# Kernel optimization log

Measured on AMD Instinct MI355X. Metric: run time of the kernel, lower is better.

## Reference

```python
import jax, jax.numpy as jnp
import numpy as np

H = 64        # hidden_dim
A = 21        # N_ACTIONS
B = 262144    # batch size


def setup_inputs() -> dict:
    key = jax.random.key(0)
    ks = jax.random.split(key, 32)

    def w(k, shape):
        fan_in = shape[0]
        return (jax.random.normal(k, shape, jnp.float32) / np.float32(np.sqrt(fan_in)))

    inp = {
        "x": jax.random.normal(ks[0], (B, 2, 2), jnp.float32),
        "b_act1": jax.random.randint(ks[1], (B,), 0, A),
        "b_act2": jax.random.randint(ks[2], (B,), 0, A),
        # enc: Linear(2,H), ReLU, Linear(H,H), ReLU
        "enc_w1": w(ks[3], (2, H)), "enc_b1": jnp.zeros((H,), jnp.float32),
        "enc_w2": w(ks[4], (H, H)), "enc_b2": jnp.zeros((H,), jnp.float32),
        # q_net: Linear(H,H), ReLU, Linear(H,A)
        "q_w1": w(ks[5], (H, H)), "q_b1": jnp.zeros((H,), jnp.float32),
        "q_w2": w(ks[6], (H, A)), "q_b2": jnp.zeros((A,), jnp.float32),
        # v_net: Linear(H,H), ReLU, Linear(H,1)
        "v_w1": w(ks[7], (H, H)), "v_b1": jnp.zeros((H,), jnp.float32),
        "v_w2": w(ks[8], (H, 1)), "v_b2": jnp.zeros((1,), jnp.float32),
        # lin2: Linear(H+A,H), ReLU, Linear(H,H), ReLU, Linear(H,H)
        "l2_w1": w(ks[9], (H + A, H)), "l2_b1": jnp.zeros((H,), jnp.float32),
        "l2_w2": w(ks[10], (H, H)), "l2_b2": jnp.zeros((H,), jnp.float32),
        "l2_w3": w(ks[11], (H, H)), "l2_b3": jnp.zeros((H,), jnp.float32),
        # lin3, lin4
        "l3_w": w(ks[12], (H, H)), "l3_b": jnp.zeros((H,), jnp.float32),
        "l4_w": w(ks[13], (H, A)), "l4_b": jnp.zeros((A,), jnp.float32),
        # q_prime_net: Linear(H,2H) ELU Linear(2H,H) ELU Linear(H,H) ELU Linear(H,1)
        "qp_w1": w(ks[14], (H, 2 * H)), "qp_b1": jnp.zeros((2 * H,), jnp.float32),
        "qp_w2": w(ks[15], (2 * H, H)), "qp_b2": jnp.zeros((H,), jnp.float32),
        "qp_w3": w(ks[16], (H, H)), "qp_b3": jnp.zeros((H,), jnp.float32),
        "qp_w4": w(ks[17], (H, 1)), "qp_b4": jnp.zeros((1,), jnp.float32),
    }
    return inp


def reference(x, b_act1, b_act2,
              enc_w1, enc_b1, enc_w2, enc_b2,
              q_w1, q_b1, q_w2, q_b2,
              v_w1, v_b1, v_w2, v_b2,
              l2_w1, l2_b1, l2_w2, l2_b2, l2_w3, l2_b3,
              l3_w, l3_b, l4_w, l4_b,
              qp_w1, qp_b1, qp_w2, qp_b2, qp_w3, qp_b3, qp_w4, qp_b4):
    relu = jax.nn.relu
    elu = jax.nn.elu

    def enc(z):
        return relu(relu(z @ enc_w1 + enc_b1) @ enc_w2 + enc_b2)

    def q_net(h):
        return relu(h @ q_w1 + q_b1) @ q_w2 + q_b2

    def lin2(e):  # ends with bare Linear (no final activation)
        h = relu(e @ l2_w1 + l2_b1)
        h = relu(h @ l2_w2 + l2_b2)
        return h @ l2_w3 + l2_b3

    def q_prime(z):
        h = elu(z @ qp_w1 + qp_b1)
        h = elu(h @ qp_w2 + qp_b2)
        h = elu(h @ qp_w3 + qp_b3)
        return h @ qp_w4 + qp_b4

    h1 = enc(x[:, 0, :])  # [B,H]
    h2 = enc(x[:, 1, :])
    q1, q2 = q_net(h1), q_net(h2)              # [B,A]
    key2 = jnp.stack([h1, h2], axis=1)          # [B,2,H]
    vtot = relu((h1 + h2) @ v_w1 + v_b1) @ v_w2 + v_b2  # [B,1]

    def joint(act1, act2):
        oh1 = jax.nn.one_hot(act1, A, dtype=h1.dtype)
        oh2 = jax.nn.one_hot(act2, A, dtype=h2.dtype)
        e = jnp.stack([jnp.concatenate([h1, oh1], axis=-1),
                       jnp.concatenate([h2, oh2], axis=-1)], axis=1)  # [B,2,H+A]
        key1 = lin2(e)                              # [B,2,H]
        q = q_prime(key1.mean(axis=1))              # [B,1]
        return key1, q

    key1, joint_qs = joint(b_act1, b_act2)
    a1_max = jnp.argmax(q1, axis=1)
    a2_max = jnp.argmax(q2, axis=1)
    key1_max, joint_max_qs = joint(a1_max, a2_max)

    def q_jt(k1):
        z = key2 + k1.mean(axis=1, keepdims=True) - k1 / 2  # [B,2,H]
        return relu(z @ l3_w + l3_b) @ l4_w + l4_b           # [B,2,A]

    q_jt_alt = q_jt(key1)
    q_jt_max_alt = q_jt(key1_max)

    return (q1, q2, joint_qs, joint_max_qs, vtot, q_jt_alt, q_jt_max_alt)
```

## Files before the change

### kernel.cpp

```cpp
#include <hip/hip_runtime.h>
#include <hip/hip_bf16.h>


#define B_TOT 262144

typedef __bf16 bf16_t;
typedef __bf16 bf16x4 __attribute__((ext_vector_type(4)));
typedef __bf16 bf16x8 __attribute__((ext_vector_type(8)));
typedef float  f32x2  __attribute__((ext_vector_type(2)));
typedef float  f32x4  __attribute__((ext_vector_type(4)));

#define MFMA16(a, b, c) __builtin_amdgcn_mfma_f32_16x16x32_bf16((a), (b), (c), 0, 0, 0)

enum : int {
  OFF_VW1  = 0,
  OFF_L2W1 = 4096,
  OFF_L2W2 = 8192,
  OFF_L2W3 = 12288,
  OFF_L3W  = 16384,
  OFF_L4W  = 20480,
  OFF_QP1  = 22528,
  OFF_QP2  = 30720,
  OFF_QP3  = 38912,
  WS_ELEMS = 43008
};
#define WS_BYTES (WS_ELEMS * 2)

enum : int {
  O_Q1   = 0,
  O_Q2   = 21 * B_TOT,
  O_JQ   = 42 * B_TOT,
  O_JMQ  = 43 * B_TOT,
  O_VT   = 44 * B_TOT,
  O_QJT  = 45 * B_TOT,
  O_QJTM = 87 * B_TOT
};

struct RDesc { const float* src; int K; int N; int NT; int off; };
struct RPack { RDesc d[9]; };

__global__ void repack_kernel(RPack P, bf16_t* __restrict__ ws) {
  RDesc d = P.d[blockIdx.x];
  int n = (d.K >> 5) * d.NT * 512;
  for (int i = threadIdx.x; i < n; i += blockDim.x) {
    int j  = i & 7;
    int l  = (i >> 3) & 63;
    int t  = i >> 9;
    int nt = t % d.NT;
    int kc = t / d.NT;
    int sk = kc * 32 + 16 * (j >> 2) + 4 * (l >> 4) + (j & 3);
    int sn = nt * 16 + (l & 15);
    float v = (sn < d.N) ? d.src[sk * d.N + sn] : 0.0f;
    ws[d.off + i] = (bf16_t)v;
  }
}

struct Args {
  const float* x; const int* a1; const int* a2;
  const float* ew1; const float* eb1; const float* ew2; const float* eb2;
  const float* qw1; const float* qb1; const float* qw2; const float* qb2;
  const float* vw1; const float* vb1; const float* vw2; const float* vb2;
  const float* l2w1; const float* l2b1; const float* l2w2; const float* l2b2;
  const float* l2w3; const float* l2b3;
  const float* l3w;  const float* l3b;  const float* l4w;  const float* l4b;
  const float* qpw1; const float* qpb1; const float* qpw2; const float* qpb2;
  const float* qpw3; const float* qpb3; const float* qpw4; const float* qpb4;
  float* out; const bf16_t* ws;
};

struct __align__(16) SMem {
  unsigned char scr[16896];
  bf16_t h1b[64 * 68];
  bf16_t h2b[64 * 68];
  float  bias[768];
  int    acts[128];
  int    amax[128];
  float  red[64][2];
  int    redi[64][2];
};

__device__ __forceinline__ float eluf(float x) { return x > 0.f ? x : expm1f(x); }

__device__ __forceinline__ void fcA64ip(float* __restrict__ f,
                                        const float* __restrict__ W,
                                        const float* __restrict__ Bv,
                                        bf16_t* __restrict__ hb, int r, int g) {
  f32x2 acc[8];
  const f32x2* Bv2 = (const f32x2*)(Bv + g * 16);
#pragma unroll
  for (int i = 0; i < 8; i++) acc[i] = Bv2[i];
  const f32x2* fr = (const f32x2*)(f + r * 66);
#pragma unroll 1
  for (int hh = 0; hh < 2; hh++) {
    f32x2 in[16];
#pragma unroll
    for (int i = 0; i < 16; i++) in[i] = fr[16 * hh + i];
#pragma unroll 4
    for (int k2 = 0; k2 < 16; k2++) {
      int k = 32 * hh + 2 * k2;
      const f32x2* wr0 = (const f32x2*)(W + k * 64 + g * 16);
      const f32x2* wr1 = (const f32x2*)(W + (k + 1) * 64 + g * 16);
      f32x2 a0 = {in[k2][0], in[k2][0]};
      f32x2 a1 = {in[k2][1], in[k2][1]};
#pragma unroll
      for (int i = 0; i < 8; i++) acc[i] += a0 * wr0[i];
#pragma unroll
      for (int i = 0; i < 8; i++) acc[i] += a1 * wr1[i];
    }
  }
  __syncthreads();
#pragma unroll
  for (int i = 0; i < 8; i++) {
    float v0 = fmaxf(acc[i][0], 0.f), v1 = fmaxf(acc[i][1], 0.f);
    f32x2 v = {v0, v1};
    *(f32x2*)(f + r * 66 + g * 16 + 2 * i) = v;
    if (hb) {
      hb[r * 68 + g * 16 + 2 * i]     = (bf16_t)v0;
      hb[r * 68 + g * 16 + 2 * i + 1] = (bf16_t)v1;
    }
  }
  __syncthreads();
}

template <int NC>
__device__ __forceinline__ void qn2(const float* __restrict__ fin, const float* __restrict__ W21,
                                    const float* __restrict__ Bv, float* __restrict__ qo,
                                    int r, int colbase, float& bv, int& bi) {
  float acc[NC];
#pragma unroll
  for (int i = 0; i < NC; i++) acc[i] = Bv[colbase + i];
  for (int k2 = 0; k2 < 32; k2++) {
    f32x2 a = *(const f32x2*)(fin + r * 66 + 2 * k2);
    const float* wr0 = W21 + (2 * k2) * 21 + colbase;
    const float* wr1 = W21 + (2 * k2 + 1) * 21 + colbase;
#pragma unroll
    for (int i = 0; i < NC; i++) acc[i] = fmaf(a[0], wr0[i], acc[i]);
#pragma unroll
    for (int i = 0; i < NC; i++) acc[i] = fmaf(a[1], wr1[i], acc[i]);
  }
  bv = -3e38f; bi = 0;
#pragma unroll
  for (int i = 0; i < NC; i++) {
    qo[i] = acc[i];
    if (acc[i] > bv) { bv = acc[i]; bi = colbase + i; }
  }
}

template <bool USEWS, int NT, int KC>
__device__ __forceinline__ f32x4 tileT(const bf16x8* __restrict__ WF,
                                       const float* __restrict__ Wp, int N, int woff,
                                       const bf16x8* __restrict__ bin,
                                       const float* __restrict__ bias, int bbase,
                                       int nt, int l, int c, int u) {
  f32x4 a = *(const f32x4*)(bias + bbase + nt * 16 + 4 * u);
#pragma unroll
  for (int kc = 0; kc < KC; kc++) {
    bf16x8 w;
    if constexpr (USEWS) {
      w = WF[(woff >> 3) + (kc * NT + nt) * 64 + l];
    } else {
      int sn = nt * 16 + c;
      if (sn < N) {
#pragma unroll
        for (int j = 0; j < 8; j++)
          w[j] = (bf16_t)Wp[(kc * 32 + 16 * (j >> 2) + 4 * u + (j & 3)) * N + sn];
      } else {
#pragma unroll
        for (int j = 0; j < 8; j++) w[j] = (bf16_t)0.0f;
      }
    }
    a = MFMA16(w, bin[kc], a);
  }
  return a;
}

template <int MODE>
__device__ __forceinline__ bf16x8 pack2(f32x4 t0, f32x4 t1) {
  bf16x8 r;
#pragma unroll
  for (int j = 0; j < 8; j++) {
    float v = (j >> 2) ? t1[j & 3] : t0[j & 3];
    if constexpr (MODE == 1) v = fmaxf(v, 0.f);
    if constexpr (MODE == 2) v = eluf(v);
    r[j] = (bf16_t)v;
  }
  return r;
}

template <bool USEWS>
__global__ __launch_bounds__(256, 3) void qtran_main(Args A) {
  __shared__ SMem sm;
  const int t = threadIdx.x;
  const int wgbase = blockIdx.x * 64;
  const int r = t & 63;
  const int g = __builtin_amdgcn_readfirstlane(t >> 6);

  float* f0 = (float*)sm.scr;

  if (t < 64) {
    sm.bias[t]        = A.vb1[t];
    sm.bias[64 + t]   = A.l2b1[t];
    sm.bias[128 + t]  = A.l2b2[t];
    sm.bias[192 + t]  = A.l2b3[t];
    sm.bias[384 + t]  = A.qpb2[t];
    sm.bias[448 + t]  = A.qpb3[t];
    sm.bias[512 + t]  = A.l3b[t];
    sm.bias[608 + t]  = A.vw2[t];
    sm.bias[672 + t]  = A.qpw4[t];
    sm.acts[t]        = A.a1[wgbase + t];
    sm.acts[64 + t]   = A.a2[wgbase + t];
  } else if (t < 192) {
    sm.bias[256 + t - 64] = A.qpb1[t - 64];
  } else if (t < 224) {
    int i = t - 192;
    sm.bias[576 + i] = (i < 21) ? A.l4b[i] : 0.0f;
  } else if (t == 224) {
    sm.bias[736] = A.vb2[0];
    sm.bias[737] = A.qpb4[0];
  }

  const int rowg = wgbase + r;
  float4 xv = ((const float4*)A.x)[rowg];
#pragma unroll 1
  for (int s = 0; s < 2; ++s) {
    float xa = s ? xv.z : xv.x;
    float xb = s ? xv.w : xv.y;
#pragma unroll
    for (int cc = 0; cc < 16; cc += 2) {
      int col = g * 16 + cc;
      float h0 = fmaf(xa, A.ew1[col],     fmaf(xb, A.ew1[64 + col],     A.eb1[col]));
      float h1 = fmaf(xa, A.ew1[col + 1], fmaf(xb, A.ew1[64 + col + 1], A.eb1[col + 1]));
      f32x2 v = {fmaxf(h0, 0.f), fmaxf(h1, 0.f)};
      *(f32x2*)(f0 + r * 66 + col) = v;
    }
    __syncthreads();
    fcA64ip(f0, A.ew2, A.eb2, s ? sm.h2b : sm.h1b, r, g);
    fcA64ip(f0, A.qw1, A.qb1, nullptr, r, g);
    {
      float* qo = A.out + (s ? O_Q2 : O_Q1) + rowg * 21;
      float bv; int bi;
      if (g == 0) {
        qn2<16>(f0, A.qw2, A.qb2, qo, r, 0, bv, bi);
        sm.red[r][0] = bv; sm.redi[r][0] = bi;
      } else if (g == 1) {
        qn2<5>(f0, A.qw2, A.qb2, qo + 16, r, 16, bv, bi);
        sm.red[r][1] = bv; sm.redi[r][1] = bi;
      }
    }
    __syncthreads();
    if (t < 64)
      sm.amax[s * 64 + t] = (sm.red[t][0] >= sm.red[t][1]) ? sm.redi[t][0] : sm.redi[t][1];
    __syncthreads();
  }

  const int l = t & 63;
  const int c = l & 15, u = l >> 4;
  const int rb = g * 16;
  const int row = rb + c;
  float* out = A.out;
  const bf16x8* WF = (const bf16x8*)A.ws;
  const float* bias = sm.bias;
  float* S = (float*)sm.scr;

  auto HG = [&](const bf16_t* __restrict__ HB, int kc) -> bf16x8 {
    const bf16_t* p = HB + row * 68 + kc * 32 + 4 * u;
    bf16x4 lo = *(const bf16x4*)p;
    bf16x4 hi = *(const bf16x4*)(p + 16);
    bf16x8 rr;
#pragma unroll
    for (int d = 0; d < 4; d++) { rr[d] = lo[d]; rr[4 + d] = hi[d]; }
    return rr;
  };

  {
    bf16x8 aS[2];
#pragma unroll
    for (int kc = 0; kc < 2; kc++) {
      bf16x8 a1 = HG(sm.h1b, kc), a2 = HG(sm.h2b, kc);
      bf16x8 s8;
#pragma unroll
      for (int i = 0; i < 8; i++) s8[i] = (bf16_t)((float)a1[i] + (float)a2[i]);
      aS[kc] = s8;
    }
    float pr = 0.f;
#pragma unroll
    for (int nt = 0; nt < 4; nt++) {
      f32x4 tv = tileT<USEWS, 4, 2>(WF, A.vw1, 64, OFF_VW1, aS, bias, 0, nt, l, c, u);
      f32x4 wv = *(const f32x4*)(bias + 608 + nt * 16 + 4 * u);
#pragma unroll
      for (int p = 0; p < 4; p++) pr += fmaxf(tv[p], 0.f) * wv[p];
    }
    pr += __shfl_xor(pr, 16, 64);
    pr += __shfl_xor(pr, 32, 64);
    if (u == 0) out[O_VT + wgbase + row] = pr + bias[736];
  }

  auto J = [&](const int* __restrict__ asrc, int jointBase, int qjtBase) {
    bf16x8 k1f[2][2];
#pragma unroll
    for (int j = 0; j < 2; j++) {
      const bf16_t* HB = j ? sm.h2b : sm.h1b;
      const int act = asrc[j * 64 + row];
      bf16x8 bh[2];
#pragma unroll
      for (int kc = 0; kc < 2; kc++) bh[kc] = HG(HB, kc);
      const float* ohp = A.l2w1 + (64 + act) * 64 + 4 * u;
      bf16x8 b1[2];
#pragma unroll
      for (int f = 0; f < 2; f++) {
        f32x4 t0 = tileT<USEWS, 4, 2>(WF, A.l2w1, 64, OFF_L2W1, bh, bias, 64, 2 * f, l, c, u);
        f32x4 t1 = tileT<USEWS, 4, 2>(WF, A.l2w1, 64, OFF_L2W1, bh, bias, 64, 2 * f + 1, l, c, u);
        t0 += *(const f32x4*)(ohp + (2 * f) * 16);
        t1 += *(const f32x4*)(ohp + (2 * f + 1) * 16);
        b1[f] = pack2<1>(t0, t1);
      }
      bf16x8 b2[2];
#pragma unroll
      for (int f = 0; f < 2; f++) {
        f32x4 t0 = tileT<USEWS, 4, 2>(WF, A.l2w2, 64, OFF_L2W2, b1, bias, 128, 2 * f, l, c, u);
        f32x4 t1 = tileT<USEWS, 4, 2>(WF, A.l2w2, 64, OFF_L2W2, b1, bias, 128, 2 * f + 1, l, c, u);
        b2[f] = pack2<1>(t0, t1);
      }
#pragma unroll
      for (int f = 0; f < 2; f++) {
        f32x4 t0 = tileT<USEWS, 4, 2>(WF, A.l2w3, 64, OFF_L2W3, b2, bias, 192, 2 * f, l, c, u);
        f32x4 t1 = tileT<USEWS, 4, 2>(WF, A.l2w3, 64, OFF_L2W3, b2, bias, 192, 2 * f + 1, l, c, u);
        k1f[j][f] = pack2<0>(t0, t1);
      }
    }
#pragma unroll
    for (int j = 0; j < 2; j++) {
      const bf16_t* HB = j ? sm.h2b : sm.h1b;
      bf16x8 aZ[2];
#pragma unroll
      for (int kc = 0; kc < 2; kc++) {
        bf16x8 h8 = HG(HB, kc);
        bf16x8 kk = k1f[1 - j][kc];
#pragma unroll
        for (int i = 0; i < 8; i++)
          aZ[kc][i] = (bf16_t)((float)h8[i] + 0.5f * (float)kk[i]);
      }
      bf16x8 bz[2];
#pragma unroll
      for (int f = 0; f < 2; f++) {
        f32x4 t0 = tileT<USEWS, 4, 2>(WF, A.l3w, 64, OFF_L3W, aZ, bias, 512, 2 * f, l, c, u);
        f32x4 t1 = tileT<USEWS, 4, 2>(WF, A.l3w, 64, OFF_L3W, aZ, bias, 512, 2 * f + 1, l, c, u);
        bz[f] = pack2<1>(t0, t1);
      }
#pragma unroll
      for (int nt = 0; nt < 2; nt++) {
        f32x4 tq = tileT<USEWS, 2, 2>(WF, A.l4w, 21, OFF_L4W, bz, bias, 576, nt, l, c, u);
#pragma unroll
        for (int p = 0; p < 4; p++) {
          int n2 = nt * 16 + 4 * u + p;
          if (n2 < 21) S[row * 43 + j * 21 + n2] = tq[p];
        }
      }
    }
    bf16x8 aM[2];
#pragma unroll
    for (int kc = 0; kc < 2; kc++)
#pragma unroll
      for (int i = 0; i < 8; i++)
        aM[kc][i] = (bf16_t)(0.5f * ((float)k1f[0][kc][i] + (float)k1f[1][kc][i]));
    {
      const int ob = qjtBase + (wgbase + rb) * 42;
      const float* Sx = S + rb * 43;
      for (int i2 = l; i2 < 672; i2 += 64)
        out[ob + i2] = Sx[(i2 / 42) * 43 + (i2 % 42)];
    }
    bf16x8 bq[4];
#pragma unroll
    for (int f = 0; f < 4; f++) {
      f32x4 t0 = tileT<USEWS, 8, 2>(WF, A.qpw1, 128, OFF_QP1, aM, bias, 256, 2 * f, l, c, u);
      f32x4 t1 = tileT<USEWS, 8, 2>(WF, A.qpw1, 128, OFF_QP1, aM, bias, 256, 2 * f + 1, l, c, u);
      bq[f] = pack2<2>(t0, t1);
    }
    bf16x8 b3[2];
#pragma unroll
    for (int f = 0; f < 2; f++) {
      f32x4 t0 = tileT<USEWS, 4, 4>(WF, A.qpw2, 64, OFF_QP2, bq, bias, 384, 2 * f, l, c, u);
      f32x4 t1 = tileT<USEWS, 4, 4>(WF, A.qpw2, 64, OFF_QP2, bq, bias, 384, 2 * f + 1, l, c, u);
      b3[f] = pack2<2>(t0, t1);
    }
    float pj = 0.f;
#pragma unroll
    for (int nt = 0; nt < 4; nt++) {
      f32x4 tq = tileT<USEWS, 4, 2>(WF, A.qpw3, 64, OFF_QP3, b3, bias, 448, nt, l, c, u);
      f32x4 w4 = *(const f32x4*)(bias + 672 + nt * 16 + 4 * u);
#pragma unroll
      for (int p = 0; p < 4; p++) pj += eluf(tq[p]) * w4[p];
    }
    pj += __shfl_xor(pj, 16, 64);
    pj += __shfl_xor(pj, 32, 64);
    if (u == 0) out[jointBase + wgbase + row] = pj + bias[737];
  };

  J(sm.acts, O_JQ, O_QJT);
  J(sm.amax, O_JMQ, O_QJTM);
}

extern "C" void kernel_launch(void* const* d_in, const int* in_sizes, int n_in,
                              void* d_out, int out_size, void* d_ws, size_t ws_size,
                              hipStream_t stream) {
  (void)in_sizes; (void)n_in; (void)out_size;
  Args A;
  A.x    = (const float*)d_in[0];
  A.a1   = (const int*)d_in[1];
  A.a2   = (const int*)d_in[2];
  A.ew1  = (const float*)d_in[3];
  A.eb1  = (const float*)d_in[4];
  A.ew2  = (const float*)d_in[5];
  A.eb2  = (const float*)d_in[6];
  A.qw1  = (const float*)d_in[7];
  A.qb1  = (const float*)d_in[8];
  A.qw2  = (const float*)d_in[9];
  A.qb2  = (const float*)d_in[10];
  A.vw1  = (const float*)d_in[11];
  A.vb1  = (const float*)d_in[12];
  A.vw2  = (const float*)d_in[13];
  A.vb2  = (const float*)d_in[14];
  A.l2w1 = (const float*)d_in[15];
  A.l2b1 = (const float*)d_in[16];
  A.l2w2 = (const float*)d_in[17];
  A.l2b2 = (const float*)d_in[18];
  A.l2w3 = (const float*)d_in[19];
  A.l2b3 = (const float*)d_in[20];
  A.l3w  = (const float*)d_in[21];
  A.l3b  = (const float*)d_in[22];
  A.l4w  = (const float*)d_in[23];
  A.l4b  = (const float*)d_in[24];
  A.qpw1 = (const float*)d_in[25];
  A.qpb1 = (const float*)d_in[26];
  A.qpw2 = (const float*)d_in[27];
  A.qpb2 = (const float*)d_in[28];
  A.qpw3 = (const float*)d_in[29];
  A.qpb3 = (const float*)d_in[30];
  A.qpw4 = (const float*)d_in[31];
  A.qpb4 = (const float*)d_in[32];
  A.out  = (float*)d_out;
  A.ws   = (const bf16_t*)d_ws;

  if (ws_size >= (size_t)WS_BYTES) {
    bf16_t* ws = (bf16_t*)d_ws;
    RPack P;
    P.d[0] = {A.vw1,  64, 64,  4, OFF_VW1};
    P.d[1] = {A.l2w1, 64, 64,  4, OFF_L2W1};
    P.d[2] = {A.l2w2, 64, 64,  4, OFF_L2W2};
    P.d[3] = {A.l2w3, 64, 64,  4, OFF_L2W3};
    P.d[4] = {A.l3w,  64, 64,  4, OFF_L3W};
    P.d[5] = {A.l4w,  64, 21,  2, OFF_L4W};
    P.d[6] = {A.qpw1, 64, 128, 8, OFF_QP1};
    P.d[7] = {A.qpw2, 128, 64, 4, OFF_QP2};
    P.d[8] = {A.qpw3, 64, 64,  4, OFF_QP3};
    hipLaunchKernelGGL(repack_kernel, dim3(9), dim3(256), 0, stream, P, ws);
    hipLaunchKernelGGL(HIP_KERNEL_NAME(qtran_main<true>), dim3(B_TOT / 64), dim3(256), 0,
                       stream, A);
  } else {
    hipLaunchKernelGGL(HIP_KERNEL_NAME(qtran_main<false>), dim3(B_TOT / 64), dim3(256), 0,
                       stream, A);
  }
}
```

Baseline: 952.3 us.

## Split q-head argmax across four wave groups, use fast exp, relax launch bounds

The q_net output head (21 actions) is now split across all four wave groups (6/5/5/5 columns) instead of two (16/5), and the per-row argmax merges four partial results. ELU switches from expm1f to __expf(x)-1, launch bounds drop from 3 to 2 blocks per CU to allow more registers, and the q_jt output copy loop replaces its divide/modulo indexing with incremental row/column counters. Together these target load imbalance, transcendental cost and integer overhead. In exchange they risk lower occupancy, slightly less accurate ELU near zero, and possible argmax tie-breaking differences.

After: 903.0 us. 1.05x faster.

```diff
diff --git a/kernel.cpp b/kernel.cpp
--- a/kernel.cpp
+++ b/kernel.cpp
@@ -75,11 +75,13 @@
   float  bias[768];
   int    acts[128];
   int    amax[128];
-  float  red[64][2];
-  int    redi[64][2];
+  float  red[64][4];
+  int    redi[64][4];
 };
 
-__device__ __forceinline__ float eluf(float x) { return x > 0.f ? x : expm1f(x); }
+__device__ __forceinline__ float eluf(float x) {
+  return x > 0.f ? x : __expf(x) - 1.0f;
+}
 
 __device__ __forceinline__ void fcA64ip(float* __restrict__ f,
                                         const float* __restrict__ W,
@@ -188,7 +190,7 @@
 }
 
 template <bool USEWS>
-__global__ __launch_bounds__(256, 3) void qtran_main(Args A) {
+__global__ __launch_bounds__(256, 2) void qtran_main(Args A) {
   __shared__ SMem sm;
   const int t = threadIdx.x;
   const int wgbase = blockIdx.x * 64;
@@ -239,17 +241,20 @@
     {
       float* qo = A.out + (s ? O_Q2 : O_Q1) + rowg * 21;
       float bv; int bi;
-      if (g == 0) {
-        qn2<16>(f0, A.qw2, A.qb2, qo, r, 0, bv, bi);
-        sm.red[r][0] = bv; sm.redi[r][0] = bi;
-      } else if (g == 1) {
-        qn2<5>(f0, A.qw2, A.qb2, qo + 16, r, 16, bv, bi);
-        sm.red[r][1] = bv; sm.redi[r][1] = bi;
-      }
+      if (g == 0)      qn2<6>(f0, A.qw2, A.qb2, qo,      r, 0,  bv, bi);
+      else if (g == 1) qn2<5>(f0, A.qw2, A.qb2, qo + 6,  r, 6,  bv, bi);
+      else if (g == 2) qn2<5>(f0, A.qw2, A.qb2, qo + 11, r, 11, bv, bi);
+      else             qn2<5>(f0, A.qw2, A.qb2, qo + 16, r, 16, bv, bi);
+      sm.red[r][g] = bv; sm.redi[r][g] = bi;
     }
     __syncthreads();
-    if (t < 64)
-      sm.amax[s * 64 + t] = (sm.red[t][0] >= sm.red[t][1]) ? sm.redi[t][0] : sm.redi[t][1];
+    if (t < 64) {
+      float b0 = sm.red[t][0]; int i0 = sm.redi[t][0];
+#pragma unroll
+      for (int grp = 1; grp < 4; grp++)
+        if (sm.red[t][grp] > b0) { b0 = sm.red[t][grp]; i0 = sm.redi[t][grp]; }
+      sm.amax[s * 64 + t] = i0;
+    }
     __syncthreads();
   }
 
@@ -366,8 +371,13 @@
     {
       const int ob = qjtBase + (wgbase + rb) * 42;
       const float* Sx = S + rb * 43;
-      for (int i2 = l; i2 < 672; i2 += 64)
-        out[ob + i2] = Sx[(i2 / 42) * 43 + (i2 % 42)];
+      int colw = l, roww = 0;
+      if (colw >= 42) { colw -= 42; roww = 1; }
+      for (int i2 = l; i2 < 672; i2 += 64) {
+        out[ob + i2] = Sx[roww * 43 + colw];
+        colw += 22; roww += 1;
+        if (colw >= 42) { colw -= 42; roww += 1; }
+      }
     }
     bf16x8 bq[4];
 #pragma unroll
```
